# Kernel tuning notes

Measured on AMD Instinct MI355X. Metric: run time of the kernel, lower is better.

Reference implementation:

```python
import jax, jax.numpy as jnp
import numpy as np

H, B, C, T, F = 4, 2, 64, 2048, 64   # n_head, batch, in_chan, time, n_freqs
HID = 4                               # hid_chan (per-head Q/K channels)
VD = C // H                           # per-head V channels
EPS = 1e-5


def prelu(x, a):
    return jnp.where(x >= 0, x, a * x)


def ln_cf(x, g, b):
    # LayerNormalization4D: normalize over (channel, freq) axes of (..., C, T, F)
    mu = x.mean(axis=(-3, -1), keepdims=True)
    var = ((x - mu) ** 2).mean(axis=(-3, -1), keepdims=True)
    return (x - mu) / jnp.sqrt(var + EPS) * g + b


def setup_inputs() -> dict:
    key = jax.random.key(0)
    ks = jax.random.split(key, 8)

    def w(k, shape):
        return jax.random.normal(k, shape, jnp.float32) * 0.05

    return {
        "x": jax.random.normal(ks[0], (B, C, T, F), jnp.float32),
        # per-head 1x1-conv Q/K/V projections (stacked over head axis)
        "Wq": w(ks[1], (H, HID, C)), "bq": jnp.zeros((H, HID), jnp.float32),
        "aq": jnp.full((H,), 0.25, jnp.float32),
        "gq": jnp.ones((H, HID, F), jnp.float32), "betq": jnp.zeros((H, HID, F), jnp.float32),
        "Wk": w(ks[2], (H, HID, C)), "bk": jnp.zeros((H, HID), jnp.float32),
        "ak": jnp.full((H,), 0.25, jnp.float32),
        "gk": jnp.ones((H, HID, F), jnp.float32), "betk": jnp.zeros((H, HID, F), jnp.float32),
        "Wv": w(ks[3], (H, VD, C)), "bv": jnp.zeros((H, VD), jnp.float32),
        "av": jnp.full((H,), 0.25, jnp.float32),
        "gv": jnp.ones((H, VD, F), jnp.float32), "betv": jnp.zeros((H, VD, F), jnp.float32),
        # output 1x1-conv projection
        "Wp": w(ks[4], (C, C)), "bp": jnp.zeros((C,), jnp.float32),
        "ap": jnp.full((), 0.25, jnp.float32),
        "gp": jnp.ones((C, F), jnp.float32), "betp": jnp.zeros((C, F), jnp.float32),
    }


def reference(x, Wq, bq, aq, gq, betq, Wk, bk, ak, gk, betk,
              Wv, bv, av, gv, betv, Wp, bp, ap, gp, betp):
    def qkv(W, b, a, g, be):
        # batched per-head 1x1 conv: (H,O,C) x (B,C,T,F) -> (H,B,O,T,F)
        y = jnp.einsum('hoc,bctf->hbotf', W, x) + b[:, None, :, None, None]
        y = prelu(y, a[:, None, None, None, None])
        return ln_cf(y, g[:, None, :, None, :], be[:, None, :, None, :])

    Q = qkv(Wq, bq, aq, gq, betq).reshape(H * B, HID, T, F)
    K = qkv(Wk, bk, ak, gk, betk).reshape(H * B, HID, T, F)
    V = qkv(Wv, bv, av, gv, betv).reshape(H * B, VD, T, F)

    # (HB, C', T, F) -> (HB, T, C'*F)
    Q = Q.transpose(0, 2, 1, 3).reshape(H * B, T, HID * F)
    K = K.transpose(0, 2, 1, 3).reshape(H * B, T, HID * F)
    V = V.transpose(0, 2, 1, 3).reshape(H * B, T, VD * F)

    scale = 1.0 / jnp.sqrt(jnp.asarray(HID * F, jnp.float32))
    attn = jax.nn.softmax(jnp.einsum('bqd,bkd->bqk', Q, K) * scale, axis=-1)  # (HB,T,T)
    O = jnp.einsum('bqk,bkd->bqd', attn, V)                                    # (HB,T,VD*F)

    # (HB,T,VD,F) -> (B, H*VD, T, F) matching torch head-concat order
    O = O.reshape(H * B, T, VD, F).transpose(0, 2, 1, 3)
    O = O.reshape(H, B, VD, T, F).transpose(1, 0, 2, 3, 4).reshape(B, H * VD, T, F)

    y = jnp.einsum('oc,bctf->botf', Wp, O) + bp[None, :, None, None]
    y = prelu(y, ap)
    y = ln_cf(y, gp[:, None, :], betp[:, None, :])
    return y + x
```

## Files before the change

### kernel.cpp

```cpp
#include <hip/hip_runtime.h>

#define EPS_ 1e-5f

typedef float f32x4 __attribute__((ext_vector_type(4)));
typedef short s16x8 __attribute__((ext_vector_type(8)));

static __device__ __forceinline__ short f2bf(float f) {
    unsigned u = __float_as_uint(f);
    unsigned r = (u + 0x7FFFu + ((u >> 16) & 1u)) >> 16;
    return (short)r;
}
static __device__ __forceinline__ float bf2f(short s) {
    return __uint_as_float(((unsigned)(unsigned short)s) << 16);
}

static __device__ __forceinline__ void gload16(const short* g, short* l) {
    __builtin_amdgcn_global_load_lds(
        (const __attribute__((address_space(1))) unsigned int*)g,
        (__attribute__((address_space(3))) unsigned int*)l, 16, 0, 0);
}

__global__ __launch_bounds__(256) void prep_kernel(
    const float* __restrict__ Wq, const float* __restrict__ Wk,
    const float* __restrict__ Wv, const float* __restrict__ Wp,
    short* __restrict__ Wbf, short* __restrict__ Wpbf)
{
    int i = blockIdx.x * 256 + threadIdx.x;
    if (i < 6144) {
        float v = (i < 1024) ? Wq[i] : (i < 2048 ? Wk[i - 1024] : Wv[i - 2048]);
        Wbf[i] = f2bf(v);
    } else if (i < 6144 + 4096) {
        Wpbf[i - 6144] = f2bf(Wp[i - 6144]);
    }
}

__global__ __launch_bounds__(256) void qkv_kernel(
    const float* __restrict__ x, const short* __restrict__ Wbf,
    const float* __restrict__ bq, const float* __restrict__ aq,
    const float* __restrict__ gq, const float* __restrict__ betq,
    const float* __restrict__ bk, const float* __restrict__ ak,
    const float* __restrict__ gk, const float* __restrict__ betk,
    const float* __restrict__ bv, const float* __restrict__ av,
    const float* __restrict__ gv, const float* __restrict__ betv,
    short* __restrict__ Qo, short* __restrict__ Ko, short* __restrict__ Vo)
{
    const int t = blockIdx.x;
    const int b = blockIdx.y;
    const int tid = threadIdx.x;
    const int wid = tid >> 6, lane = tid & 63;
    const int g = lane >> 4, c16 = lane & 15;
    const int f_ = tid & 63, cg = tid >> 6;

    __shared__ __align__(16) short wlds[96 * 64];
    __shared__ __align__(16) short xs[64 * 64];
    __shared__ float zs[96 * 64];
    __shared__ float stats[12][2];
    __shared__ float bias_l[96], alpha_l[96];

#pragma unroll
    for (int j = 0; j < 3; ++j) {
        int i8 = tid + 256 * j;
        int row = i8 >> 3, cb = i8 & 7;
        s16x8 v = *(const s16x8*)(Wbf + i8 * 8);
        *(s16x8*)&wlds[row * 64 + ((cb ^ (row & 7)) * 8)] = v;
    }
    if (tid < 96) {
        int row = tid; float bias, al;
        if (row < 16)      { bias = bq[row];      al = aq[row >> 2]; }
        else if (row < 32) { bias = bk[row - 16]; al = ak[(row - 16) >> 2]; }
        else               { bias = bv[row - 32]; al = av[(row - 32) >> 4]; }
        bias_l[row] = bias; alpha_l[row] = al;
    }
#pragma unroll
    for (int it = 0; it < 2; ++it) {
        int cb = cg + 4 * it, c0 = cb * 8;
        s16x8 v;
#pragma unroll
        for (int i = 0; i < 8; ++i)
            v[i] = f2bf(x[(((size_t)b * 64 + c0 + i) * 2048 + t) * 64 + f_]);
        *(s16x8*)&xs[f_ * 64 + ((cb ^ (f_ & 7)) * 8)] = v;
    }
    __syncthreads();

    const int f0 = wid * 16;
    s16x8 bfr[2];
#pragma unroll
    for (int kk = 0; kk < 2; ++kk)
        bfr[kk] = *(const s16x8*)&xs[(f0 + c16) * 64 + (((kk * 4 + g) ^ (c16 & 7)) * 8)];

    f32x4 acc[6];
#pragma unroll
    for (int rt = 0; rt < 6; ++rt) {
#pragma unroll
        for (int r = 0; r < 4; ++r) acc[rt][r] = 0.f;
#pragma unroll
        for (int kk = 0; kk < 2; ++kk) {
            s16x8 a = *(const s16x8*)&wlds[(rt * 16 + c16) * 64 + (((kk * 4 + g) ^ (c16 & 7)) * 8)];
            acc[rt] = __builtin_amdgcn_mfma_f32_16x16x32_bf16(a, bfr[kk], acc[rt], 0, 0, 0);
        }
    }

#pragma unroll
    for (int rt = 0; rt < 6; ++rt)
#pragma unroll
        for (int r = 0; r < 4; ++r) {
            int row = rt * 16 + g * 4 + r;
            float z = acc[rt][r] + bias_l[row];
            z = z >= 0.f ? z : alpha_l[row] * z;
            zs[row * 64 + f0 + c16] = z;
        }
    __syncthreads();

#pragma unroll
    for (int gi = 0; gi < 3; ++gi) {
        int grp = wid * 3 + gi;
        int base_row, n;
        if (grp < 4)      { base_row = grp * 4;             n = 256; }
        else if (grp < 8) { base_row = 16 + (grp - 4) * 4;  n = 256; }
        else              { base_row = 32 + (grp - 8) * 16; n = 1024; }
        int cnt = n >> 6;
        float s = 0.f, ss = 0.f;
        for (int i = 0; i < cnt; ++i) {
            float v = zs[(base_row + i) * 64 + lane];
            s += v; ss += v * v;
        }
#pragma unroll
        for (int msk = 32; msk >= 1; msk >>= 1) {
            s  += __shfl_xor(s, msk);
            ss += __shfl_xor(ss, msk);
        }
        if (lane == 0) {
            float mean = s / n;
            float var = ss / n - mean * mean;
            stats[grp][0] = mean;
            stats[grp][1] = rsqrtf(var + EPS_);
        }
    }
    __syncthreads();

#pragma unroll
    for (int j = 0; j < 24; ++j) {
        int row = cg + 4 * j;
        float zv = zs[row * 64 + f_];
        if (row < 16) {
            int grp = row >> 2;
            float val = (zv - stats[grp][0]) * stats[grp][1];
            val = val * gq[row * 64 + f_] + betq[row * 64 + f_];
            int h = row >> 2, o = row & 3;
            Qo[(((size_t)(h * 2 + b)) * 2048 + t) * 256 + o * 64 + f_] = f2bf(val);
        } else if (row < 32) {
            int rr = row - 16, grp = 4 + (rr >> 2);
            float val = (zv - stats[grp][0]) * stats[grp][1];
            val = val * gk[rr * 64 + f_] + betk[rr * 64 + f_];
            int h = rr >> 2, o = rr & 3;
            Ko[(((size_t)(h * 2 + b)) * 2048 + t) * 256 + o * 64 + f_] = f2bf(val);
        } else {
            int rr = row - 32, grp = 8 + (rr >> 4);
            float val = (zv - stats[grp][0]) * stats[grp][1];
            val = val * gv[rr * 64 + f_] + betv[rr * 64 + f_];
            int h = rr >> 4, ov = rr & 15;
            Vo[(((size_t)(h * 2 + b)) * 2048 + t) * 1024 + ov * 64 + f_] = f2bf(val);
        }
    }
}

__global__ __launch_bounds__(256) void vtrans_kernel(
    const short* __restrict__ Vrm, short* __restrict__ Vt)
{
    const int t0 = blockIdx.x * 64;
    const int d0 = blockIdx.y * 64;
    const int hb = blockIdx.z;
    const int tid = threadIdx.x;
    __shared__ __align__(16) short tile[64 * 72];

#pragma unroll
    for (int k = 0; k < 2; ++k) {
        int q = tid + 256 * k;
        int row = q >> 3, slot = q & 7;
        s16x8 v = *(const s16x8*)(Vrm + ((size_t)hb * 2048 + t0 + row) * 1024 + d0 + slot * 8);
        *(s16x8*)&tile[row * 72 + slot * 8] = v;
    }
    __syncthreads();
#pragma unroll
    for (int k = 0; k < 2; ++k) {
        int q = tid + 256 * k;
        int drow = q >> 3, tslot = q & 7;
        s16x8 v;
#pragma unroll
        for (int i = 0; i < 8; ++i)
            v[i] = tile[(tslot * 8 + i) * 72 + drow];
        *(s16x8*)(Vt + ((size_t)hb * 1024 + d0 + drow) * 2048 + t0 + tslot * 8) = v;
    }
}

__global__ __launch_bounds__(512, 2) void attn_kernel(
    const short* __restrict__ Qg, const short* __restrict__ Kg,
    const short* __restrict__ Vt, short* __restrict__ Ob)
{
    const int hb = blockIdx.x;
    const int qt = blockIdx.y;
    const int dh = blockIdx.z;
    const int t0 = qt * 64;
    const int tid = threadIdx.x;
    const int lane = tid & 63;
    const int wid = tid >> 6;
    const int qs = wid >> 1;
    const int kp = wid & 1;
    const int g = lane >> 4, c16 = lane & 15;

    __shared__ __align__(16) short k_lds[64 * 256];
    __shared__ __align__(16) short p_lds[64 * 68];
    __shared__ float lpart[2][64];

    const size_t kgbase = (size_t)hb * 2048 * 256;
    const int dsl = dh * 512 + wid * 64;
    const size_t vrow0 = (size_t)hb * 1024 + dsl + c16;

    const size_t qbase = ((size_t)hb * 2048 + t0 + qs * 16 + c16) * 256;
    s16x8 qf[8];
#pragma unroll
    for (int kf = 0; kf < 8; ++kf)
        qf[kf] = *(const s16x8*)(Qg + qbase + kf * 32 + g * 8);

    f32x4 oacc[16];
#pragma unroll
    for (int i = 0; i < 16; ++i)
#pragma unroll
        for (int r = 0; r < 4; ++r) oacc[i][r] = 0.f;

    float l_r[4] = {0.f, 0.f, 0.f, 0.f};

#define STAGE_K(kt) do {                                                       \
    _Pragma("unroll")                                                          \
    for (int j_ = 0; j_ < 4; ++j_) {                                           \
        int c_ = (wid * 4 + j_) * 64 + lane;                                   \
        int row_ = c_ >> 5, sp_ = c_ & 31;                                     \
        int slot_ = sp_ ^ (row_ & 7);                                          \
        gload16(Kg + kgbase + (size_t)((kt) * 64 + row_) * 256 + slot_ * 8,    \
                &k_lds[(wid * 4 + j_) * 512]);                                 \
    }                                                                          \
} while (0)

    STAGE_K(0);
    __syncthreads();

    for (int t = 0; t < 32; ++t) {
        const int kt0 = t * 64;

        s16x8 vf[4][2];
#pragma unroll
        for (int dt = 0; dt < 4; ++dt)
#pragma unroll
            for (int ks = 0; ks < 2; ++ks)
                vf[dt][ks] = *(const s16x8*)(Vt + (vrow0 + dt * 16) * 2048 + kt0 + (ks * 4 + g) * 8);

        f32x4 sf[2];
#pragma unroll
        for (int nf = 0; nf < 2; ++nf)
#pragma unroll
            for (int r = 0; r < 4; ++r) sf[nf][r] = 0.f;
        __builtin_amdgcn_s_setprio(1);
#pragma unroll
        for (int kf = 0; kf < 8; ++kf) {
#pragma unroll
            for (int nf = 0; nf < 2; ++nf) {
                int krow = kp * 32 + nf * 16 + c16;
                s16x8 kb = *(const s16x8*)&k_lds[krow * 256 + (((kf * 4 + g) ^ (krow & 7)) * 8)];
                sf[nf] = __builtin_amdgcn_mfma_f32_16x16x32_bf16(qf[kf], kb, sf[nf], 0, 0, 0);
            }
        }
        __builtin_amdgcn_s_setprio(0);

        float rs[4] = {0.f, 0.f, 0.f, 0.f};
#pragma unroll
        for (int nf = 0; nf < 2; ++nf)
#pragma unroll
            for (int r = 0; r < 4; ++r) {
                float p = __expf(sf[nf][r] * 0.0625f);
                sf[nf][r] = p;
                rs[r] += p;
            }
#pragma unroll
        for (int msk = 1; msk <= 8; msk <<= 1)
#pragma unroll
            for (int r = 0; r < 4; ++r) rs[r] += __shfl_xor(rs[r], msk);
#pragma unroll
        for (int r = 0; r < 4; ++r) l_r[r] += rs[r];

#pragma unroll
        for (int nf = 0; nf < 2; ++nf)
#pragma unroll
            for (int r = 0; r < 4; ++r)
                p_lds[(qs * 16 + g * 4 + r) * 68 + kp * 32 + nf * 16 + c16] = f2bf(sf[nf][r]);

        __syncthreads();

        if (t < 31) STAGE_K(t + 1);

        s16x8 pa[4][2];
#pragma unroll
        for (int s4 = 0; s4 < 4; ++s4)
#pragma unroll
            for (int ks = 0; ks < 2; ++ks)
                pa[s4][ks] = *(const s16x8*)&p_lds[(s4 * 16 + c16) * 68 + ks * 32 + g * 8];

        __builtin_amdgcn_s_setprio(1);
#pragma unroll
        for (int dt = 0; dt < 4; ++dt)
#pragma unroll
            for (int s4 = 0; s4 < 4; ++s4)
#pragma unroll
                for (int ks = 0; ks < 2; ++ks)
                    oacc[dt * 4 + s4] = __builtin_amdgcn_mfma_f32_16x16x32_bf16(
                        pa[s4][ks], vf[dt][ks], oacc[dt * 4 + s4], 0, 0, 0);
        __builtin_amdgcn_s_setprio(0);

        __syncthreads();
    }

#undef STAGE_K

    if (c16 == 0) {
#pragma unroll
        for (int r = 0; r < 4; ++r)
            lpart[kp][qs * 16 + g * 4 + r] = l_r[r];
    }
    __syncthreads();

    float li[16];
#pragma unroll
    for (int s4 = 0; s4 < 4; ++s4)
#pragma unroll
        for (int r = 0; r < 4; ++r) {
            int row = s4 * 16 + g * 4 + r;
            li[s4 * 4 + r] = 1.f / (lpart[0][row] + lpart[1][row]);
        }

    const int h = hb >> 1, b = hb & 1;
#pragma unroll
    for (int dt = 0; dt < 4; ++dt) {
        int vcol = dsl + dt * 16 + c16;
        int cout = h * 16 + (vcol >> 6), ff = vcol & 63;
#pragma unroll
        for (int s4 = 0; s4 < 4; ++s4)
#pragma unroll
            for (int r = 0; r < 4; ++r) {
                int trow = t0 + s4 * 16 + g * 4 + r;
                Ob[(((size_t)b * 64 + cout) * 2048 + trow) * 64 + ff] =
                    f2bf(oacc[dt * 4 + s4][r] * li[s4 * 4 + r]);
            }
    }
}

__global__ __launch_bounds__(256) void oproj_kernel(
    const short* __restrict__ Ob, const float* __restrict__ x,
    const short* __restrict__ Wpbf,
    const float* __restrict__ bp, const float* __restrict__ ap,
    const float* __restrict__ gp, const float* __restrict__ betp,
    float* __restrict__ out)
{
    const int t = blockIdx.x;
    const int b = blockIdx.y;
    const int tid = threadIdx.x;
    const int wid = tid >> 6, lane = tid & 63;
    const int g = lane >> 4, c16 = lane & 15;
    const int f_ = tid & 63, cg = tid >> 6;

    __shared__ __align__(16) short wp[64 * 64];
    __shared__ __align__(16) short os[64 * 64];
    __shared__ float zs[64 * 64];
    __shared__ float red[4][2];

#pragma unroll
    for (int j = 0; j < 2; ++j) {
        int i8 = tid + 256 * j;
        int row = i8 >> 3, cb = i8 & 7;
        s16x8 v = *(const s16x8*)(Wpbf + i8 * 8);
        *(s16x8*)&wp[row * 64 + ((cb ^ (row & 7)) * 8)] = v;
    }
#pragma unroll
    for (int it = 0; it < 2; ++it) {
        int cb = cg + 4 * it, c0 = cb * 8;
        s16x8 v;
#pragma unroll
        for (int i = 0; i < 8; ++i)
            v[i] = Ob[(((size_t)b * 64 + c0 + i) * 2048 + t) * 64 + f_];
        *(s16x8*)&os[f_ * 64 + ((cb ^ (f_ & 7)) * 8)] = v;
    }
    __syncthreads();

    const int f0 = wid * 16;
    s16x8 bfr[2];
#pragma unroll
    for (int kk = 0; kk < 2; ++kk)
        bfr[kk] = *(const s16x8*)&os[(f0 + c16) * 64 + (((kk * 4 + g) ^ (c16 & 7)) * 8)];

    const float ap0 = ap[0];
    f32x4 acc[4];
#pragma unroll
    for (int rt = 0; rt < 4; ++rt) {
#pragma unroll
        for (int r = 0; r < 4; ++r) acc[rt][r] = 0.f;
#pragma unroll
        for (int kk = 0; kk < 2; ++kk) {
            s16x8 a = *(const s16x8*)&wp[(rt * 16 + c16) * 64 + (((kk * 4 + g) ^ (c16 & 7)) * 8)];
            acc[rt] = __builtin_amdgcn_mfma_f32_16x16x32_bf16(a, bfr[kk], acc[rt], 0, 0, 0);
        }
    }

#pragma unroll
    for (int rt = 0; rt < 4; ++rt)
#pragma unroll
        for (int r = 0; r < 4; ++r) {
            int row = rt * 16 + g * 4 + r;
            float z = acc[rt][r] + bp[row];
            z = z >= 0.f ? z : ap0 * z;
            zs[row * 64 + f0 + c16] = z;
        }
    __syncthreads();

    float s = 0.f, ss = 0.f;
#pragma unroll
    for (int j = 0; j < 16; ++j) {
        float v = zs[(cg + 4 * j) * 64 + f_];
        s += v; ss += v * v;
    }
#pragma unroll
    for (int msk = 32; msk >= 1; msk >>= 1) {
        s  += __shfl_xor(s, msk);
        ss += __shfl_xor(ss, msk);
    }
    if (lane == 0) { red[wid][0] = s; red[wid][1] = ss; }
    __syncthreads();
    float ts  = red[0][0] + red[1][0] + red[2][0] + red[3][0];
    float tss = red[0][1] + red[1][1] + red[2][1] + red[3][1];
    float mean = ts * (1.f / 4096.f);
    float rstd = rsqrtf(tss * (1.f / 4096.f) - mean * mean + EPS_);

#pragma unroll
    for (int j = 0; j < 16; ++j) {
        int row = cg + 4 * j;
        size_t idx = (((size_t)b * 64 + row) * 2048 + t) * 64 + f_;
        out[idx] = (zs[row * 64 + f_] - mean) * rstd * gp[row * 64 + f_]
                 + betp[row * 64 + f_] + x[idx];
    }
}

extern "C" void kernel_launch(void* const* d_in, const int* in_sizes, int n_in,
                              void* d_out, int out_size, void* d_ws, size_t ws_size,
                              hipStream_t stream)
{
    const float* x    = (const float*)d_in[0];
    const float* Wq   = (const float*)d_in[1];
    const float* bq   = (const float*)d_in[2];
    const float* aq   = (const float*)d_in[3];
    const float* gq   = (const float*)d_in[4];
    const float* betq = (const float*)d_in[5];
    const float* Wk   = (const float*)d_in[6];
    const float* bk   = (const float*)d_in[7];
    const float* ak   = (const float*)d_in[8];
    const float* gk   = (const float*)d_in[9];
    const float* betk = (const float*)d_in[10];
    const float* Wv   = (const float*)d_in[11];
    const float* bv   = (const float*)d_in[12];
    const float* av   = (const float*)d_in[13];
    const float* gv   = (const float*)d_in[14];
    const float* betv = (const float*)d_in[15];
    const float* Wp   = (const float*)d_in[16];
    const float* bp   = (const float*)d_in[17];
    const float* ap   = (const float*)d_in[18];
    const float* gp   = (const float*)d_in[19];
    const float* betp = (const float*)d_in[20];

    short* Qb   = (short*)d_ws;
    short* Kb   = Qb   + (size_t)8 * 2048 * 256;
    short* Vrm  = Kb   + (size_t)8 * 2048 * 256;
    short* Vt   = Vrm  + (size_t)8 * 2048 * 1024;
    short* Obuf = Vt   + (size_t)8 * 2048 * 1024;
    short* Wbf  = Obuf + (size_t)8 * 2048 * 1024;
    short* Wpbf = Wbf  + 96 * 64;

    prep_kernel<<<40, 256, 0, stream>>>(Wq, Wk, Wv, Wp, Wbf, Wpbf);
    qkv_kernel<<<dim3(2048, 2), 256, 0, stream>>>(x, Wbf,
        bq, aq, gq, betq, bk, ak, gk, betk, bv, av, gv, betv, Qb, Kb, Vrm);
    vtrans_kernel<<<dim3(32, 16, 8), 256, 0, stream>>>(Vrm, Vt);
    attn_kernel<<<dim3(8, 32, 2), 512, 0, stream>>>(Qb, Kb, Vt, Obuf);
    oproj_kernel<<<dim3(2048, 2), 256, 0, stream>>>(Obuf, x, Wpbf,
        bp, ap, gp, betp, (float*)d_out);
}
```

Before: 280.9 us.

## Restructure attention so each wave keeps its own P in registers

Each of the 8 waves now owns 16 query rows (128 per block) and computes S transposed (K as the A operand), so the softmax probabilities land in register layout usable directly as the A operand of the PV MFMA. This removes the P round-trip through LDS and one barrier per iteration. Vt is permuted in the transpose kernel to match that register layout. K staging is double-buffered and issued ahead, and V fragments stream through a two-slot register pipeline across 32 output tiles. The cost is a 128-register accumulator per wave and half as many blocks in the grid, which risks register pressure and lower occupancy.

```diff
diff --git a/kernel.cpp b/kernel.cpp
--- a/kernel.cpp
+++ b/kernel.cpp
@@ -187,8 +187,11 @@
         int drow = q >> 3, tslot = q & 7;
         s16x8 v;
 #pragma unroll
-        for (int i = 0; i < 8; ++i)
-            v[i] = tile[(tslot * 8 + i) * 72 + drow];
+        for (int i = 0; i < 8; ++i) {
+            int src = ((tslot >> 2) & 1) * 32 + ((i >> 2) & 1) * 16
+                    + ((tslot >> 1) & 1) * 8 + (tslot & 1) * 4 + (i & 3);
+            v[i] = tile[src * 72 + drow];
+        }
         *(s16x8*)(Vt + ((size_t)hb * 1024 + d0 + drow) * 2048 + t0 + tslot * 8) = v;
     }
 }
@@ -200,155 +203,146 @@
     const int hb = blockIdx.x;
     const int qt = blockIdx.y;
     const int dh = blockIdx.z;
-    const int t0 = qt * 64;
+    const int t0 = qt * 128;
     const int tid = threadIdx.x;
     const int lane = tid & 63;
-    const int wid = tid >> 6;
-    const int qs = wid >> 1;
-    const int kp = wid & 1;
+    const int wq = tid >> 6;
     const int g = lane >> 4, c16 = lane & 15;
 
-    __shared__ __align__(16) short k_lds[64 * 256];
-    __shared__ __align__(16) short p_lds[64 * 68];
-    __shared__ float lpart[2][64];
+    __shared__ __align__(16) short k_lds[2][64 * 256];
 
     const size_t kgbase = (size_t)hb * 2048 * 256;
-    const int dsl = dh * 512 + wid * 64;
-    const size_t vrow0 = (size_t)hb * 1024 + dsl + c16;
-
-    const size_t qbase = ((size_t)hb * 2048 + t0 + qs * 16 + c16) * 256;
+    const size_t vbase = (size_t)hb * 1024 + dh * 512;
+    const int swz = c16 & 7;
+
+    const size_t qrow = (size_t)hb * 2048 + t0 + wq * 16 + c16;
     s16x8 qf[8];
 #pragma unroll
     for (int kf = 0; kf < 8; ++kf)
-        qf[kf] = *(const s16x8*)(Qg + qbase + kf * 32 + g * 8);
-
-    f32x4 oacc[16];
-#pragma unroll
-    for (int i = 0; i < 16; ++i)
+        qf[kf] = *(const s16x8*)(Qg + qrow * 256 + kf * 32 + g * 8);
+
+    f32x4 oacc[32];
+#pragma unroll
+    for (int i = 0; i < 32; ++i)
 #pragma unroll
         for (int r = 0; r < 4; ++r) oacc[i][r] = 0.f;
 
-    float l_r[4] = {0.f, 0.f, 0.f, 0.f};
-
-#define STAGE_K(kt) do {                                                       \
+    float l_r = 0.f;
+
+#define STAGE_K(buf, kt) do {                                                  \
     _Pragma("unroll")                                                          \
     for (int j_ = 0; j_ < 4; ++j_) {                                           \
-        int c_ = (wid * 4 + j_) * 64 + lane;                                   \
+        int c_ = (wq * 4 + j_) * 64 + lane;                                    \
         int row_ = c_ >> 5, sp_ = c_ & 31;                                     \
         int slot_ = sp_ ^ (row_ & 7);                                          \
         gload16(Kg + kgbase + (size_t)((kt) * 64 + row_) * 256 + slot_ * 8,    \
-                &k_lds[(wid * 4 + j_) * 512]);                                 \
+                &k_lds[buf][(wq * 4 + j_) * 512]);                             \
     }                                                                          \
 } while (0)
 
-    STAGE_K(0);
+    STAGE_K(0, 0);
     __syncthreads();
 
     for (int t = 0; t < 32; ++t) {
         const int kt0 = t * 64;
 
-        s16x8 vf[4][2];
-#pragma unroll
-        for (int dt = 0; dt < 4; ++dt)
-#pragma unroll
-            for (int ks = 0; ks < 2; ++ks)
-                vf[dt][ks] = *(const s16x8*)(Vt + (vrow0 + dt * 16) * 2048 + kt0 + (ks * 4 + g) * 8);
-
-        f32x4 sf[2];
-#pragma unroll
-        for (int nf = 0; nf < 2; ++nf)
-#pragma unroll
-            for (int r = 0; r < 4; ++r) sf[nf][r] = 0.f;
+        s16x8 vr[2][4][2];
+#pragma unroll
+        for (int d4 = 0; d4 < 4; ++d4)
+#pragma unroll
+            for (int s = 0; s < 2; ++s)
+                vr[0][d4][s] = *(const s16x8*)(Vt + (vbase + d4 * 16 + c16) * 2048
+                                               + kt0 + s * 32 + g * 8);
+
+        if (t < 31) STAGE_K((t + 1) & 1, t + 1);
+
+        f32x4 sf[4];
+#pragma unroll
+        for (int kt = 0; kt < 4; ++kt)
+#pragma unroll
+            for (int r = 0; r < 4; ++r) sf[kt][r] = 0.f;
         __builtin_amdgcn_s_setprio(1);
 #pragma unroll
         for (int kf = 0; kf < 8; ++kf) {
 #pragma unroll
-            for (int nf = 0; nf < 2; ++nf) {
-                int krow = kp * 32 + nf * 16 + c16;
-                s16x8 kb = *(const s16x8*)&k_lds[krow * 256 + (((kf * 4 + g) ^ (krow & 7)) * 8)];
-                sf[nf] = __builtin_amdgcn_mfma_f32_16x16x32_bf16(qf[kf], kb, sf[nf], 0, 0, 0);
+            for (int kt = 0; kt < 4; ++kt) {
+                s16x8 kb = *(const s16x8*)&k_lds[t & 1]
+                    [(kt * 16 + c16) * 256 + (((kf * 4 + g) ^ swz) * 8)];
+                sf[kt] = __builtin_amdgcn_mfma_f32_16x16x32_bf16(kb, qf[kf], sf[kt], 0, 0, 0);
             }
         }
         __builtin_amdgcn_s_setprio(0);
 
-        float rs[4] = {0.f, 0.f, 0.f, 0.f};
-#pragma unroll
-        for (int nf = 0; nf < 2; ++nf)
+        float rs = 0.f;
+#pragma unroll
+        for (int kt = 0; kt < 4; ++kt)
 #pragma unroll
             for (int r = 0; r < 4; ++r) {
-                float p = __expf(sf[nf][r] * 0.0625f);
-                sf[nf][r] = p;
-                rs[r] += p;
+                float p = __expf(sf[kt][r] * 0.0625f);
+                sf[kt][r] = p;
+                rs += p;
             }
-#pragma unroll
-        for (int msk = 1; msk <= 8; msk <<= 1)
-#pragma unroll
-            for (int r = 0; r < 4; ++r) rs[r] += __shfl_xor(rs[r], msk);
-#pragma unroll
-        for (int r = 0; r < 4; ++r) l_r[r] += rs[r];
-
-#pragma unroll
-        for (int nf = 0; nf < 2; ++nf)
-#pragma unroll
-            for (int r = 0; r < 4; ++r)
-                p_lds[(qs * 16 + g * 4 + r) * 68 + kp * 32 + nf * 16 + c16] = f2bf(sf[nf][r]);
-
-        __syncthreads();
-
-        if (t < 31) STAGE_K(t + 1);
-
-        s16x8 pa[4][2];
-#pragma unroll
-        for (int s4 = 0; s4 < 4; ++s4)
-#pragma unroll
-            for (int ks = 0; ks < 2; ++ks)
-                pa[s4][ks] = *(const s16x8*)&p_lds[(s4 * 16 + c16) * 68 + ks * 32 + g * 8];
-
-        __builtin_amdgcn_s_setprio(1);
-#pragma unroll
-        for (int dt = 0; dt < 4; ++dt)
-#pragma unroll
-            for (int s4 = 0; s4 < 4; ++s4)
-#pragma unroll
-                for (int ks = 0; ks < 2; ++ks)
-                    oacc[dt * 4 + s4] = __builtin_amdgcn_mfma_f32_16x16x32_bf16(
-                        pa[s4][ks], vf[dt][ks], oacc[dt * 4 + s4], 0, 0, 0);
-        __builtin_amdgcn_s_setprio(0);
-
-        __syncthreads();
+        rs += __shfl_xor(rs, 16);
+        rs += __shfl_xor(rs, 32);
+        l_r += rs;
+
+        s16x8 pa0, pa1;
+#pragma unroll
+        for (int e = 0; e < 8; ++e) {
+            pa0[e] = f2bf(sf[(e >> 2)][e & 3]);
+            pa1[e] = f2bf(sf[2 + (e >> 2)][e & 3]);
+        }
+
+#pragma unroll
+        for (int d4 = 0; d4 < 4; ++d4)
+#pragma unroll
+            for (int s = 0; s < 2; ++s)
+                vr[1][d4][s] = *(const s16x8*)(Vt + (vbase + (4 + d4) * 16 + c16) * 2048
+                                               + kt0 + s * 32 + g * 8);
+
+#pragma unroll
+        for (int bat = 0; bat < 8; ++bat) {
+            __builtin_amdgcn_s_setprio(1);
+#pragma unroll
+            for (int d4 = 0; d4 < 4; ++d4) {
+                oacc[bat * 4 + d4] = __builtin_amdgcn_mfma_f32_16x16x32_bf16(
+                    pa0, vr[bat & 1][d4][0], oacc[bat * 4 + d4], 0, 0, 0);
+                oacc[bat * 4 + d4] = __builtin_amdgcn_mfma_f32_16x16x32_bf16(
+                    pa1, vr[bat & 1][d4][1], oacc[bat * 4 + d4], 0, 0, 0);
+            }
+            __builtin_amdgcn_s_setprio(0);
+            if (bat < 6) {
+#pragma unroll
+                for (int d4 = 0; d4 < 4; ++d4)
+#pragma unroll
+                    for (int s = 0; s < 2; ++s)
+                        vr[bat & 1][d4][s] = *(const s16x8*)(Vt
+                            + (vbase + ((bat + 2) * 4 + d4) * 16 + c16) * 2048
+                            + kt0 + s * 32 + g * 8);
+            }
+        }
+
+        if (t < 31) __syncthreads();
     }
 
 #undef STAGE_K
 
-    if (c16 == 0) {
-#pragma unroll
-        for (int r = 0; r < 4; ++r)
-            lpart[kp][qs * 16 + g * 4 + r] = l_r[r];
-    }
-    __syncthreads();
-
-    float li[16];
-#pragma unroll
-    for (int s4 = 0; s4 < 4; ++s4)
+    float li[4];
+#pragma unroll
+    for (int r = 0; r < 4; ++r)
+        li[r] = 1.f / __shfl(l_r, g * 4 + r);
+
+    const int h = hb >> 1, b = hb & 1;
+#pragma unroll
+    for (int dt = 0; dt < 32; ++dt) {
+        int vcol = dh * 512 + dt * 16 + c16;
+        int cout = h * 16 + (vcol >> 6), ff = vcol & 63;
 #pragma unroll
         for (int r = 0; r < 4; ++r) {
-            int row = s4 * 16 + g * 4 + r;
-            li[s4 * 4 + r] = 1.f / (lpart[0][row] + lpart[1][row]);
-        }
-
-    const int h = hb >> 1, b = hb & 1;
-#pragma unroll
-    for (int dt = 0; dt < 4; ++dt) {
-        int vcol = dsl + dt * 16 + c16;
-        int cout = h * 16 + (vcol >> 6), ff = vcol & 63;
-#pragma unroll
-        for (int s4 = 0; s4 < 4; ++s4)
-#pragma unroll
-            for (int r = 0; r < 4; ++r) {
-                int trow = t0 + s4 * 16 + g * 4 + r;
-                Ob[(((size_t)b * 64 + cout) * 2048 + trow) * 64 + ff] =
-                    f2bf(oacc[dt * 4 + s4][r] * li[s4 * 4 + r]);
-            }
+            int trow = t0 + wq * 16 + g * 4 + r;
+            Ob[(((size_t)b * 64 + cout) * 2048 + trow) * 64 + ff] =
+                f2bf(oacc[dt][r] * li[r]);
+        }
     }
 }
 
@@ -484,7 +478,7 @@
     qkv_kernel<<<dim3(2048, 2), 256, 0, stream>>>(x, Wbf,
         bq, aq, gq, betq, bk, ak, gk, betk, bv, av, gv, betv, Qb, Kb, Vrm);
     vtrans_kernel<<<dim3(32, 16, 8), 256, 0, stream>>>(Vrm, Vt);
-    attn_kernel<<<dim3(8, 32, 2), 512, 0, stream>>>(Qb, Kb, Vt, Obuf);
+    attn_kernel<<<dim3(8, 16, 2), 512, 0, stream>>>(Qb, Kb, Vt, Obuf);
     oproj_kernel<<<dim3(2048, 2), 256, 0, stream>>>(Obuf, x, Wpbf,
         bp, ap, gp, betp, (float*)d_out);
 }
```

Measured after the change: 661.9 us. +135.6%, slower.

## Split attention into 4 D-quarters with 256-thread blocks and no key split

Applied to the files above, without the earlier changes.

The attention kernel moves from 512-thread blocks, where warps split keys into two halves and each covers half the V columns, to 256-thread blocks over four D-quarters. Each warp now owns a 16-row query slice across all 64 keys, which removes the cross-warp row-sum merge. V fragments are loaded after the QK MFMAs and double-buffered inside the PV loop to cut register pressure. The catch is that QK^T and the softmax are recomputed four times per query tile instead of twice.

```diff
diff --git a/kernel.cpp b/kernel.cpp
--- a/kernel.cpp
+++ b/kernel.cpp
@@ -193,30 +193,28 @@
     }
 }
 
-__global__ __launch_bounds__(512, 2) void attn_kernel(
+__global__ __launch_bounds__(256, 3) void attn_kernel(
     const short* __restrict__ Qg, const short* __restrict__ Kg,
     const short* __restrict__ Vt, short* __restrict__ Ob)
 {
     const int hb = blockIdx.x;
     const int qt = blockIdx.y;
-    const int dh = blockIdx.z;
+    const int dq = blockIdx.z;
     const int t0 = qt * 64;
     const int tid = threadIdx.x;
     const int lane = tid & 63;
     const int wid = tid >> 6;
-    const int qs = wid >> 1;
-    const int kp = wid & 1;
     const int g = lane >> 4, c16 = lane & 15;
 
     __shared__ __align__(16) short k_lds[64 * 256];
-    __shared__ __align__(16) short p_lds[64 * 68];
-    __shared__ float lpart[2][64];
+    __shared__ __align__(16) short p_lds[64 * 66];
+    __shared__ float l_sh[64];
 
     const size_t kgbase = (size_t)hb * 2048 * 256;
-    const int dsl = dh * 512 + wid * 64;
+    const int dsl = dq * 256 + wid * 64;
     const size_t vrow0 = (size_t)hb * 1024 + dsl + c16;
 
-    const size_t qbase = ((size_t)hb * 2048 + t0 + qs * 16 + c16) * 256;
+    const size_t qbase = ((size_t)hb * 2048 + t0 + wid * 16 + c16) * 256;
     s16x8 qf[8];
 #pragma unroll
     for (int kf = 0; kf < 8; ++kf)
@@ -232,12 +230,12 @@
 
 #define STAGE_K(kt) do {                                                       \
     _Pragma("unroll")                                                          \
-    for (int j_ = 0; j_ < 4; ++j_) {                                           \
-        int c_ = (wid * 4 + j_) * 64 + lane;                                   \
+    for (int j_ = 0; j_ < 8; ++j_) {                                           \
+        int c_ = (wid * 8 + j_) * 64 + lane;                                   \
         int row_ = c_ >> 5, sp_ = c_ & 31;                                     \
         int slot_ = sp_ ^ (row_ & 7);                                          \
         gload16(Kg + kgbase + (size_t)((kt) * 64 + row_) * 256 + slot_ * 8,    \
-                &k_lds[(wid * 4 + j_) * 512]);                                 \
+                &k_lds[(wid * 8 + j_) * 512]);                                 \
     }                                                                          \
 } while (0)
 
@@ -247,33 +245,33 @@
     for (int t = 0; t < 32; ++t) {
         const int kt0 = t * 64;
 
-        s16x8 vf[4][2];
-#pragma unroll
-        for (int dt = 0; dt < 4; ++dt)
-#pragma unroll
-            for (int ks = 0; ks < 2; ++ks)
-                vf[dt][ks] = *(const s16x8*)(Vt + (vrow0 + dt * 16) * 2048 + kt0 + (ks * 4 + g) * 8);
-
-        f32x4 sf[2];
-#pragma unroll
-        for (int nf = 0; nf < 2; ++nf)
+        f32x4 sf[4];
+#pragma unroll
+        for (int nf = 0; nf < 4; ++nf)
 #pragma unroll
             for (int r = 0; r < 4; ++r) sf[nf][r] = 0.f;
         __builtin_amdgcn_s_setprio(1);
 #pragma unroll
         for (int kf = 0; kf < 8; ++kf) {
 #pragma unroll
-            for (int nf = 0; nf < 2; ++nf) {
-                int krow = kp * 32 + nf * 16 + c16;
+            for (int nf = 0; nf < 4; ++nf) {
+                int krow = nf * 16 + c16;
                 s16x8 kb = *(const s16x8*)&k_lds[krow * 256 + (((kf * 4 + g) ^ (krow & 7)) * 8)];
                 sf[nf] = __builtin_amdgcn_mfma_f32_16x16x32_bf16(qf[kf], kb, sf[nf], 0, 0, 0);
             }
         }
         __builtin_amdgcn_s_setprio(0);
 
+        s16x8 vf[2][2];
+#pragma unroll
+        for (int dt = 0; dt < 2; ++dt)
+#pragma unroll
+            for (int ks = 0; ks < 2; ++ks)
+                vf[dt][ks] = *(const s16x8*)(Vt + (vrow0 + dt * 16) * 2048 + kt0 + (ks * 4 + g) * 8);
+
         float rs[4] = {0.f, 0.f, 0.f, 0.f};
 #pragma unroll
-        for (int nf = 0; nf < 2; ++nf)
+        for (int nf = 0; nf < 4; ++nf)
 #pragma unroll
             for (int r = 0; r < 4; ++r) {
                 float p = __expf(sf[nf][r] * 0.0625f);
@@ -288,10 +286,10 @@
         for (int r = 0; r < 4; ++r) l_r[r] += rs[r];
 
 #pragma unroll
-        for (int nf = 0; nf < 2; ++nf)
+        for (int nf = 0; nf < 4; ++nf)
 #pragma unroll
             for (int r = 0; r < 4; ++r)
-                p_lds[(qs * 16 + g * 4 + r) * 68 + kp * 32 + nf * 16 + c16] = f2bf(sf[nf][r]);
+                p_lds[(wid * 16 + g * 4 + r) * 66 + nf * 16 + c16] = f2bf(sf[nf][r]);
 
         __syncthreads();
 
@@ -299,21 +297,27 @@
 
         s16x8 pa[4][2];
 #pragma unroll
-        for (int s4 = 0; s4 < 4; ++s4)
+        for (int qs2 = 0; qs2 < 4; ++qs2)
 #pragma unroll
             for (int ks = 0; ks < 2; ++ks)
-                pa[s4][ks] = *(const s16x8*)&p_lds[(s4 * 16 + c16) * 68 + ks * 32 + g * 8];
-
-        __builtin_amdgcn_s_setprio(1);
-#pragma unroll
-        for (int dt = 0; dt < 4; ++dt)
-#pragma unroll
-            for (int s4 = 0; s4 < 4; ++s4)
+                pa[qs2][ks] = *(const s16x8*)&p_lds[(qs2 * 16 + c16) * 66 + ks * 32 + g * 8];
+
+#pragma unroll
+        for (int dt = 0; dt < 4; ++dt) {
+            __builtin_amdgcn_s_setprio(1);
+#pragma unroll
+            for (int qs2 = 0; qs2 < 4; ++qs2)
 #pragma unroll
                 for (int ks = 0; ks < 2; ++ks)
-                    oacc[dt * 4 + s4] = __builtin_amdgcn_mfma_f32_16x16x32_bf16(
-                        pa[s4][ks], vf[dt][ks], oacc[dt * 4 + s4], 0, 0, 0);
-        __builtin_amdgcn_s_setprio(0);
+                    oacc[dt * 4 + qs2] = __builtin_amdgcn_mfma_f32_16x16x32_bf16(
+                        pa[qs2][ks], vf[dt & 1][ks], oacc[dt * 4 + qs2], 0, 0, 0);
+            __builtin_amdgcn_s_setprio(0);
+            if (dt < 2) {
+#pragma unroll
+                for (int ks = 0; ks < 2; ++ks)
+                    vf[dt & 1][ks] = *(const s16x8*)(Vt + (vrow0 + (dt + 2) * 16) * 2048 + kt0 + (ks * 4 + g) * 8);
+            }
+        }
 
         __syncthreads();
     }
@@ -323,18 +327,16 @@
     if (c16 == 0) {
 #pragma unroll
         for (int r = 0; r < 4; ++r)
-            lpart[kp][qs * 16 + g * 4 + r] = l_r[r];
+            l_sh[wid * 16 + g * 4 + r] = l_r[r];
     }
     __syncthreads();
 
     float li[16];
 #pragma unroll
-    for (int s4 = 0; s4 < 4; ++s4)
-#pragma unroll
-        for (int r = 0; r < 4; ++r) {
-            int row = s4 * 16 + g * 4 + r;
-            li[s4 * 4 + r] = 1.f / (lpart[0][row] + lpart[1][row]);
-        }
+    for (int qs2 = 0; qs2 < 4; ++qs2)
+#pragma unroll
+        for (int r = 0; r < 4; ++r)
+            li[qs2 * 4 + r] = 1.f / l_sh[qs2 * 16 + g * 4 + r];
 
     const int h = hb >> 1, b = hb & 1;
 #pragma unroll
@@ -342,12 +344,12 @@
         int vcol = dsl + dt * 16 + c16;
         int cout = h * 16 + (vcol >> 6), ff = vcol & 63;
 #pragma unroll
-        for (int s4 = 0; s4 < 4; ++s4)
+        for (int qs2 = 0; qs2 < 4; ++qs2)
 #pragma unroll
             for (int r = 0; r < 4; ++r) {
-                int trow = t0 + s4 * 16 + g * 4 + r;
+                int trow = t0 + qs2 * 16 + g * 4 + r;
                 Ob[(((size_t)b * 64 + cout) * 2048 + trow) * 64 + ff] =
-                    f2bf(oacc[dt * 4 + s4][r] * li[s4 * 4 + r]);
+                    f2bf(oacc[dt * 4 + qs2][r] * li[qs2 * 4 + r]);
             }
     }
 }
@@ -484,7 +486,7 @@
     qkv_kernel<<<dim3(2048, 2), 256, 0, stream>>>(x, Wbf,
         bq, aq, gq, betq, bk, ak, gk, betk, bv, av, gv, betv, Qb, Kb, Vrm);
     vtrans_kernel<<<dim3(32, 16, 8), 256, 0, stream>>>(Vrm, Vt);
-    attn_kernel<<<dim3(8, 32, 2), 512, 0, stream>>>(Qb, Kb, Vt, Obuf);
+    attn_kernel<<<dim3(8, 32, 4), 256, 0, stream>>>(Qb, Kb, Vt, Obuf);
     oproj_kernel<<<dim3(2048, 2), 256, 0, stream>>>(Obuf, x, Wpbf,
         bp, ap, gp, betp, (float*)d_out);
 }
```

After: 490.8 us. 74.7% more time.
